# Kernel optimization log

Hardware: AMD Instinct MI355X
Metric: run time of the kernel (lower is better)

## Reference

```python
import jax, jax.numpy as jnp
import numpy as np

DIM = 256
GROUPS = 32
EPS = 1e-6


def setup_inputs() -> dict:
    key = jax.random.key(0)
    ks = jax.random.split(key, 7)
    B, C, H, W = 4, DIM, 64, 64
    s = 1.0 / np.sqrt(C)
    return {
        "x": jax.random.normal(ks[0], (B, C, H, W), dtype=jnp.float32),
        "gamma": jnp.ones((C,), dtype=jnp.float32),
        "beta": jnp.zeros((C,), dtype=jnp.float32),
        "w_qkv": jax.random.normal(ks[1], (3 * C, C), dtype=jnp.float32) * s,
        "b_qkv": jnp.zeros((3 * C,), dtype=jnp.float32),
        "w_proj": jax.random.normal(ks[2], (C, C), dtype=jnp.float32) * s,
        "b_proj": jnp.zeros((C,), dtype=jnp.float32),
    }


def reference(x, gamma, beta, w_qkv, b_qkv, w_proj, b_proj):
    B, C, H, W = x.shape
    N = H * W
    scale = jnp.asarray(C, x.dtype) ** 0.5

    # GroupNorm(32, C, eps=1e-6, affine)
    h = x.reshape(B, GROUPS, C // GROUPS, N)
    mu = h.mean(axis=(2, 3), keepdims=True)
    var = h.var(axis=(2, 3), keepdims=True)
    h = (h - mu) * jax.lax.rsqrt(var + EPS)
    h = h.reshape(B, C, N) * gamma[None, :, None] + beta[None, :, None]

    # 1x1 conv QKV == channel matmul
    qkv = jnp.einsum('oc,bcn->bon', w_qkv, h) + b_qkv[None, :, None]  # (B,3C,N)
    qkv = qkv.reshape(B, 3, C, N)
    q = qkv[:, 0].transpose(0, 2, 1)  # (B,N,C)
    k = qkv[:, 1].transpose(0, 2, 1)
    v = qkv[:, 2].transpose(0, 2, 1)

    attn = jnp.einsum('bqc,bkc->bqk', q, k) / scale  # (B,N,N)
    attn = jax.nn.softmax(attn, axis=-1)
    out = jnp.einsum('bqk,bkc->bqc', attn, v)  # (B,N,C)

    out = out.transpose(0, 2, 1)  # (B,C,N)
    out = jnp.einsum('oc,bcn->bon', w_proj, out) + b_proj[None, :, None]
    return x + out.reshape(B, C, H, W)
```

## Files before the change

kernel.cpp:

```cpp
#include <hip/hip_runtime.h>
#include <stdint.h>

#define DIM 256
#define NPOS 4096
#define NB 4
#define GROUPS 32

typedef __attribute__((ext_vector_type(8))) short short8;
typedef __attribute__((ext_vector_type(4))) short short4v;
typedef __attribute__((ext_vector_type(4))) float f32x4;
typedef __attribute__((ext_vector_type(2))) unsigned int u32x2;

__device__ __forceinline__ short f2b(float f) {
  unsigned u = __float_as_uint(f);
  unsigned r = (u + 0x7fffu + ((u >> 16) & 1u)) >> 16;
  return (short)r;
}

__global__ void k_convert_w(const float* __restrict__ wq, const float* __restrict__ wp,
                            short* __restrict__ wqb, short* __restrict__ wpb) {
  int i = blockIdx.x * 256 + threadIdx.x;
  if (i < 768 * 256) wqb[i] = f2b(wq[i]);
  if (i < 256 * 256) wpb[i] = f2b(wp[i]);
}

__global__ void k_gn_stats(const float* __restrict__ x, float* __restrict__ stats) {
  int bg = blockIdx.x;
  const float4* b4 = (const float4*)(x + (size_t)bg * 8 * NPOS);
  float s = 0.f, ss = 0.f;
  for (int i = threadIdx.x; i < 8192; i += 256) {
    float4 v = b4[i];
    s  += v.x + v.y + v.z + v.w;
    ss += v.x * v.x + v.y * v.y + v.z * v.z + v.w * v.w;
  }
  #pragma unroll
  for (int m = 1; m < 64; m <<= 1) { s += __shfl_xor(s, m, 64); ss += __shfl_xor(ss, m, 64); }
  __shared__ float red[8];
  int wid = threadIdx.x >> 6;
  if ((threadIdx.x & 63) == 0) { red[wid * 2] = s; red[wid * 2 + 1] = ss; }
  __syncthreads();
  if (threadIdx.x == 0) {
    float S = red[0] + red[2] + red[4] + red[6];
    float SS = red[1] + red[3] + red[5] + red[7];
    float mean = S / 32768.f;
    float var = SS / 32768.f - mean * mean;
    stats[bg * 2] = mean;
    stats[bg * 2 + 1] = rsqrtf(var + 1e-6f);
  }
}

__global__ void k_gn_apply(const float* __restrict__ x, const float* __restrict__ stats,
                           const float* __restrict__ gamma, const float* __restrict__ beta,
                           short* __restrict__ ht) {
  int ct = blockIdx.x, nt = blockIdx.y, b = blockIdx.z;
  int c0 = ct * 64, n0 = nt * 64;
  __shared__ short lt[64 * 72];
  int t = threadIdx.x;
  #pragma unroll
  for (int p = 0; p < 4; ++p) {
    int row = (t >> 4) + p * 16;
    int colb = (t & 15) * 4;
    int c = c0 + row;
    float mean = stats[(b * GROUPS + (c >> 3)) * 2];
    float rstd = stats[(b * GROUPS + (c >> 3)) * 2 + 1];
    float ga = gamma[c], be = beta[c];
    float4 v = *(const float4*)(x + ((size_t)(b * DIM + c)) * NPOS + n0 + colb);
    short4v o;
    o.x = f2b((v.x - mean) * rstd * ga + be);
    o.y = f2b((v.y - mean) * rstd * ga + be);
    o.z = f2b((v.z - mean) * rstd * ga + be);
    o.w = f2b((v.w - mean) * rstd * ga + be);
    *(short4v*)&lt[row * 72 + colb] = o;
  }
  __syncthreads();
  #pragma unroll
  for (int p = 0; p < 2; ++p) {
    int nr = (t >> 3) + p * 32;
    int ch = t & 7;
    short8 o;
    #pragma unroll
    for (int j = 0; j < 8; ++j) o[j] = lt[(ch * 8 + j) * 72 + nr];
    *(short8*)(ht + ((size_t)(b * NPOS + n0 + nr)) * DIM + c0 + ch * 8) = o;
  }
}

template <int MODE>
__launch_bounds__(256, 2)
__global__ void k_gemm(const short* __restrict__ A, const short* __restrict__ Bm,
                       const float* __restrict__ bias,
                       short* __restrict__ qb, short* __restrict__ kb, short* __restrict__ vtb,
                       const float* __restrict__ resid, float* __restrict__ outf) {
  const int K = 256;
  int b = blockIdx.z;
  int m0 = blockIdx.x * 128, n0 = blockIdx.y * 128;
  const short* Ap = (MODE == 0) ? A + (size_t)b * NPOS * K : A;
  const short* Bp = (MODE == 0) ? Bm : Bm + (size_t)b * NPOS * K;

  __shared__ short As[128 * 64], Bs[128 * 64];
  int t = threadIdx.x;
  int lane = t & 63, wid = t >> 6;
  int wm = wid >> 1, wn = wid & 1;
  f32x4 acc[4][4] = {};

  for (int kt = 0; kt < 4; ++kt) {
    int k0 = kt * 64;
    short8 av[4], bv[4];
    #pragma unroll
    for (int p = 0; p < 4; ++p) {
      int ci = t + p * 256;
      int row = ci >> 3, ch = ci & 7;
      av[p] = *(const short8*)(Ap + (size_t)(m0 + row) * K + k0 + ch * 8);
      bv[p] = *(const short8*)(Bp + (size_t)(n0 + row) * K + k0 + ch * 8);
    }
    __syncthreads();
    #pragma unroll
    for (int p = 0; p < 4; ++p) {
      int ci = t + p * 256;
      int row = ci >> 3, ch = ci & 7;
      int off = (row * 128 + ch * 16) ^ ((row & 7) << 4);
      *(short8*)((char*)As + off) = av[p];
      *(short8*)((char*)Bs + off) = bv[p];
    }
    __syncthreads();
    #pragma unroll
    for (int ks = 0; ks < 2; ++ks) {
      short8 af[4], bf[4];
      int inner = ks * 64 + (lane >> 4) * 16;
      #pragma unroll
      for (int mi = 0; mi < 4; ++mi) {
        int row = wm * 64 + mi * 16 + (lane & 15);
        af[mi] = *(short8*)((char*)As + ((row * 128 + inner) ^ ((row & 7) << 4)));
      }
      #pragma unroll
      for (int ni = 0; ni < 4; ++ni) {
        int row = wn * 64 + ni * 16 + (lane & 15);
        bf[ni] = *(short8*)((char*)Bs + ((row * 128 + inner) ^ ((row & 7) << 4)));
      }
      #pragma unroll
      for (int mi = 0; mi < 4; ++mi)
        #pragma unroll
        for (int ni = 0; ni < 4; ++ni)
          acc[mi][ni] = __builtin_amdgcn_mfma_f32_16x16x32_bf16(af[mi], bf[ni], acc[mi][ni], 0, 0, 0);
    }
  }

  #pragma unroll
  for (int mi = 0; mi < 4; ++mi)
    #pragma unroll
    for (int ni = 0; ni < 4; ++ni) {
      int gcol = n0 + wn * 64 + ni * 16 + (lane & 15);
      #pragma unroll
      for (int r = 0; r < 4; ++r) {
        int grow = m0 + wm * 64 + mi * 16 + (lane >> 4) * 4 + r;
        if (MODE == 0) {
          float v = acc[mi][ni][r] + bias[gcol];
          short h = f2b(v);
          if (gcol < 256)       qb[((size_t)b * NPOS + grow) * DIM + gcol] = h;
          else if (gcol < 512)  kb[((size_t)b * NPOS + grow) * DIM + gcol - 256] = h;
          else                  vtb[((size_t)b * DIM + gcol - 512) * NPOS + grow] = h;
        } else {
          float v = acc[mi][ni][r] + bias[grow];
          size_t idx = ((size_t)b * DIM + grow) * NPOS + gcol;
          outf[idx] = v + resid[idx];
        }
      }
    }
}

__launch_bounds__(256, 2)
__global__ void k_flash(const short* __restrict__ qb, const short* __restrict__ kb,
                        const short* __restrict__ vtb, short* __restrict__ ob) {
  __shared__ __align__(16) char smem[79360];

  int i = blockIdx.x;
  int xcd = i & 7, slot = i >> 3;
  int b = xcd >> 1;
  int bx = slot * 2 + (xcd & 1);
  int q0 = bx * 32;

  int t = threadIdx.x, lane = t & 63, g = lane >> 4, wid = t >> 6;
  int qs = wid & 1, h = wid >> 1;

  const short* kbB = kb + (size_t)b * NPOS * DIM;
  const short* vbB = vtb + (size_t)b * DIM * NPOS;

  short8 qf[8];
  {
    int qrow = q0 + qs * 16 + (lane & 15);
    const short* qp = qb + ((size_t)b * NPOS + qrow) * DIM + g * 8;
    #pragma unroll
    for (int s = 0; s < 8; ++s) {
      short8 v = *(const short8*)(qp + s * 32);
      #pragma unroll
      for (int j = 0; j < 8; ++j) {
        float f = __uint_as_float(((unsigned)(unsigned short)v[j]) << 16) * 0.0625f;
        v[j] = f2b(f);
      }
      qf[s] = v;
    }
  }

  const short* A0 = kbB + (t >> 5) * 256 + (t & 31) * 8;
  const short* B0 = vbB + (t >> 2) * 4096 + (t & 3) * 8;

  int krd = h * 16896 + (lane & 15) * 528 + g * 16;
  int vrd = 33792 + h * 20480 + (lane & 15) * 80 + g * 16;
  char* prow = smem + 74752 + wid * 1024 + (lane & 15) * 64;
  float* lm = (float*)(smem + 78848);
  float* scratch = (float*)smem;

  int kwr = (t >> 5) * 528 + (t & 31) * 16;
  int vwr = 33792 + (t >> 2) * 80 + (t & 3) * 16;

  f32x4 oacc[16] = {};
  float m = -1e30f, l = 0.f;

  short8 st[16];
  #pragma unroll
  for (int p = 0; p < 16; ++p) {
    int seg = p >> 2, pp = p & 3;
    if (seg < 2) st[p] = *(const short8*)(A0 + seg * 524288 + pp * 2048);
    else         st[p] = *(const short8*)(B0 + pp * 262144 + (seg - 2) * 2048);
  }

  const int NIT = 64;
  for (int it = 0; it < NIT; ++it) {
    __syncthreads();
    #pragma unroll
    for (int p = 0; p < 16; ++p) {
      int seg = p >> 2, pp = p & 3;
      if (seg < 2) *(short8*)(smem + seg * 16896 + pp * 4224 + kwr) = st[p];
      else         *(short8*)(smem + (seg - 2) * 20480 + pp * 5120 + vwr) = st[p];
    }
    __syncthreads();
    if (it + 1 < NIT) {
      #pragma unroll
      for (int p = 0; p < 16; ++p) {
        int seg = p >> 2, pp = p & 3;
        if (seg < 2) st[p] = *(const short8*)(A0 + seg * 524288 + pp * 2048 + (it + 1) * 8192);
        else         st[p] = *(const short8*)(B0 + pp * 262144 + (seg - 2) * 2048 + (it + 1) * 32);
      }
    }

    f32x4 sacc[2] = {};
    #pragma unroll
    for (int s = 0; s < 8; ++s) {
      #pragma unroll
      for (int t2 = 0; t2 < 2; ++t2) {
        short8 kf = *(short8*)(smem + krd + t2 * 8448 + s * 64);
        sacc[t2] = __builtin_amdgcn_mfma_f32_16x16x32_bf16(kf, qf[s], sacc[t2], 0, 0, 0);
      }
    }

    float mx = fmaxf(fmaxf(fmaxf(sacc[0][0], sacc[0][1]), fmaxf(sacc[0][2], sacc[0][3])),
                     fmaxf(fmaxf(sacc[1][0], sacc[1][1]), fmaxf(sacc[1][2], sacc[1][3])));
    mx = fmaxf(mx, __shfl_xor(mx, 16, 64));
    mx = fmaxf(mx, __shfl_xor(mx, 32, 64));
    if (!__all(mx <= m + 8.f)) {
      float mn = fmaxf(m, mx);
      float al = __expf(m - mn);
      m = mn; l *= al;
      #pragma unroll
      for (int r = 0; r < 4; ++r) {
        float ar = __shfl(al, (lane & 48) + ((lane & 48) >> 2) + r, 64);
        #pragma unroll
        for (int nt = 0; nt < 16; ++nt) oacc[nt][r] *= ar;
      }
    }
    float p0 = __expf(sacc[0][0] - m), p1 = __expf(sacc[0][1] - m);
    float p2 = __expf(sacc[0][2] - m), p3 = __expf(sacc[0][3] - m);
    float p4 = __expf(sacc[1][0] - m), p5 = __expf(sacc[1][1] - m);
    float p6 = __expf(sacc[1][2] - m), p7 = __expf(sacc[1][3] - m);
    float ts = ((p0 + p1) + (p2 + p3)) + ((p4 + p5) + (p6 + p7));
    ts += __shfl_xor(ts, 16, 64);
    ts += __shfl_xor(ts, 32, 64);
    l += ts;

    unsigned w0, w1, w2, w3;
    asm("v_cvt_pk_bf16_f32 %0, %1, %2" : "=v"(w0) : "v"(p0), "v"(p1));
    asm("v_cvt_pk_bf16_f32 %0, %1, %2" : "=v"(w1) : "v"(p2), "v"(p3));
    asm("v_cvt_pk_bf16_f32 %0, %1, %2" : "=v"(w2) : "v"(p4), "v"(p5));
    asm("v_cvt_pk_bf16_f32 %0, %1, %2" : "=v"(w3) : "v"(p6), "v"(p7));
    *(short4v*)(prow + g * 8)      = __builtin_bit_cast(short4v, (u32x2){w0, w1});
    *(short4v*)(prow + 32 + g * 8) = __builtin_bit_cast(short4v, (u32x2){w2, w3});
    asm volatile("" ::: "memory");

    short8 pa = *(short8*)(prow + g * 16);
    #pragma unroll
    for (int nt = 0; nt < 16; ++nt) {
      short8 vf = *(short8*)(smem + vrd + nt * 1280);
      oacc[nt] = __builtin_amdgcn_mfma_f32_16x16x32_bf16(pa, vf, oacc[nt], 0, 0, 0);
    }
  }

  __syncthreads();
  if (lane < 16) { lm[wid * 32 + lane * 2] = m; lm[wid * 32 + lane * 2 + 1] = l; }
  __syncthreads();
  int pw = wid ^ 2;
  float mo = lm[pw * 32 + (lane & 15) * 2];
  float lo = lm[pw * 32 + (lane & 15) * 2 + 1];
  float M = fmaxf(m, mo);
  float al = __expf(m - M);
  float Lf = l * al + lo * __expf(mo - M);
  float alr[4], iLr[4];
  #pragma unroll
  for (int r = 0; r < 4; ++r) {
    int src = (lane & 48) + ((lane & 48) >> 2) + r;
    alr[r] = __shfl(al, src, 64);
    iLr[r] = 1.f / __shfl(Lf, src, 64);
  }
  __syncthreads();
  if (h == 0) {
    float* sc = scratch + qs * 4096;
    #pragma unroll
    for (int nt = 0; nt < 16; ++nt)
      #pragma unroll
      for (int r = 0; r < 4; ++r) {
        int q = 4 * g + r;
        int col = nt * 16 + (lane & 15);
        sc[(q * 256 + col) ^ ((g & 1) << 4)] = oacc[nt][r] * alr[r];
      }
  }
  __syncthreads();
  if (h == 1) {
    float* sc = scratch + qs * 4096;
    #pragma unroll
    for (int nt = 0; nt < 16; ++nt)
      #pragma unroll
      for (int r = 0; r < 4; ++r) {
        int q = 4 * g + r;
        int col = nt * 16 + (lane & 15);
        float v = (sc[(q * 256 + col) ^ ((g & 1) << 4)] + oacc[nt][r] * alr[r]) * iLr[r];
        ob[((size_t)b * NPOS + q0 + qs * 16 + q) * DIM + col] = f2b(v);
      }
  }
}

extern "C" void kernel_launch(void* const* d_in, const int* in_sizes, int n_in,
                              void* d_out, int out_size, void* d_ws, size_t ws_size,
                              hipStream_t stream) {
  const float* x     = (const float*)d_in[0];
  const float* gamma = (const float*)d_in[1];
  const float* beta  = (const float*)d_in[2];
  const float* wqkv  = (const float*)d_in[3];
  const float* bqkv  = (const float*)d_in[4];
  const float* wproj = (const float*)d_in[5];
  const float* bproj = (const float*)d_in[6];
  float* out = (float*)d_out;

  char* ws = (char*)d_ws;
  float* stats = (float*)ws;
  short* wqb = (short*)(ws + 1024);
  short* wpb = (short*)(ws + 1024 + 393216);
  size_t off = 1024 + 393216 + 131072;
  const size_t SZ = (size_t)NB * NPOS * DIM * sizeof(short);
  short* ht   = (short*)(ws + off); off += SZ;
  short* qbuf = (short*)(ws + off); off += SZ;
  short* kbuf = (short*)(ws + off); off += SZ;
  short* vtb  = (short*)(ws + off); off += SZ;
  short* obuf = ht;

  k_convert_w<<<768, 256, 0, stream>>>(wqkv, wproj, wqb, wpb);
  k_gn_stats<<<128, 256, 0, stream>>>(x, stats);
  k_gn_apply<<<dim3(4, 64, NB), 256, 0, stream>>>(x, stats, gamma, beta, ht);
  k_gemm<0><<<dim3(32, 6, NB), 256, 0, stream>>>(ht, wqb, bqkv, qbuf, kbuf, vtb, nullptr, nullptr);
  k_flash<<<dim3(512), 256, 0, stream>>>(qbuf, kbuf, vtb, obuf);
  k_gemm<1><<<dim3(2, 32, NB), 256, 0, stream>>>(wpb, obuf, bproj, nullptr, nullptr, nullptr, x, out);
}
```

Baseline: 217.6 us.

## Load K/V fragments directly from global memory instead of staging through LDS

Drops the shared-memory staging of K and V tiles, along with the register prefetch and the two barriers per iteration. Each wave now reads its MFMA operand fragments for K and transposed V straight from global memory. This shrinks LDS use and removes barrier stalls, but loses the cross-wave reuse and the software prefetch. The loads become strided (16-byte pieces per row), and latency is hidden only by occupancy and the compiler's scheduling.

```diff
diff --git a/kernel.cpp b/kernel.cpp
--- a/kernel.cpp
+++ b/kernel.cpp
@@ -170,7 +170,9 @@
 __launch_bounds__(256, 2)
 __global__ void k_flash(const short* __restrict__ qb, const short* __restrict__ kb,
                         const short* __restrict__ vtb, short* __restrict__ ob) {
-  __shared__ __align__(16) char smem[79360];
+  __shared__ __align__(16) char smem[37376];
+  float* lm = (float*)(smem + 4096);
+  float* scratch = (float*)(smem + 4608);
 
   int i = blockIdx.x;
   int xcd = i & 7, slot = i >> 3;
@@ -200,56 +202,35 @@
     }
   }
 
-  const short* A0 = kbB + (t >> 5) * 256 + (t & 31) * 8;
-  const short* B0 = vbB + (t >> 2) * 4096 + (t & 3) * 8;
-
-  int krd = h * 16896 + (lane & 15) * 528 + g * 16;
-  int vrd = 33792 + h * 20480 + (lane & 15) * 80 + g * 16;
-  char* prow = smem + 74752 + wid * 1024 + (lane & 15) * 64;
-  float* lm = (float*)(smem + 78848);
-  float* scratch = (float*)smem;
-
-  int kwr = (t >> 5) * 528 + (t & 31) * 16;
-  int vwr = 33792 + (t >> 2) * 80 + (t & 3) * 16;
+  const short* kL = kbB + ((size_t)(h * 2048 + (lane & 15))) * DIM + g * 8;
+  const short* vL = vbB + ((size_t)(lane & 15)) * NPOS + h * 2048 + g * 8;
+  char* prow = smem + wid * 1024 + (lane & 15) * 64;
 
   f32x4 oacc[16] = {};
   float m = -1e30f, l = 0.f;
 
-  short8 st[16];
-  #pragma unroll
-  for (int p = 0; p < 16; ++p) {
-    int seg = p >> 2, pp = p & 3;
-    if (seg < 2) st[p] = *(const short8*)(A0 + seg * 524288 + pp * 2048);
-    else         st[p] = *(const short8*)(B0 + pp * 262144 + (seg - 2) * 2048);
-  }
-
   const int NIT = 64;
   for (int it = 0; it < NIT; ++it) {
-    __syncthreads();
-    #pragma unroll
-    for (int p = 0; p < 16; ++p) {
-      int seg = p >> 2, pp = p & 3;
-      if (seg < 2) *(short8*)(smem + seg * 16896 + pp * 4224 + kwr) = st[p];
-      else         *(short8*)(smem + (seg - 2) * 20480 + pp * 5120 + vwr) = st[p];
-    }
-    __syncthreads();
-    if (it + 1 < NIT) {
-      #pragma unroll
-      for (int p = 0; p < 16; ++p) {
-        int seg = p >> 2, pp = p & 3;
-        if (seg < 2) st[p] = *(const short8*)(A0 + seg * 524288 + pp * 2048 + (it + 1) * 8192);
-        else         st[p] = *(const short8*)(B0 + pp * 262144 + (seg - 2) * 2048 + (it + 1) * 32);
-      }
-    }
+    int kv0 = it * 32;
+
+    short8 kf[2][8];
+    #pragma unroll
+    for (int t2 = 0; t2 < 2; ++t2)
+      #pragma unroll
+      for (int s = 0; s < 8; ++s)
+        kf[t2][s] = *(const short8*)(kL + (size_t)(kv0 + t2 * 16) * DIM + s * 32);
+
+    short8 vf[16];
+    #pragma unroll
+    for (int nt = 0; nt < 16; ++nt)
+      vf[nt] = *(const short8*)(vL + (size_t)(nt * 16) * NPOS + kv0);
 
     f32x4 sacc[2] = {};
     #pragma unroll
     for (int s = 0; s < 8; ++s) {
       #pragma unroll
-      for (int t2 = 0; t2 < 2; ++t2) {
-        short8 kf = *(short8*)(smem + krd + t2 * 8448 + s * 64);
-        sacc[t2] = __builtin_amdgcn_mfma_f32_16x16x32_bf16(kf, qf[s], sacc[t2], 0, 0, 0);
-      }
+      for (int t2 = 0; t2 < 2; ++t2)
+        sacc[t2] = __builtin_amdgcn_mfma_f32_16x16x32_bf16(kf[t2][s], qf[s], sacc[t2], 0, 0, 0);
     }
 
     float mx = fmaxf(fmaxf(fmaxf(sacc[0][0], sacc[0][1]), fmaxf(sacc[0][2], sacc[0][3])),
@@ -287,10 +268,8 @@
 
     short8 pa = *(short8*)(prow + g * 16);
     #pragma unroll
-    for (int nt = 0; nt < 16; ++nt) {
-      short8 vf = *(short8*)(smem + vrd + nt * 1280);
-      oacc[nt] = __builtin_amdgcn_mfma_f32_16x16x32_bf16(pa, vf, oacc[nt], 0, 0, 0);
-    }
+    for (int nt = 0; nt < 16; ++nt)
+      oacc[nt] = __builtin_amdgcn_mfma_f32_16x16x32_bf16(pa, vf[nt], oacc[nt], 0, 0, 0);
   }
 
   __syncthreads();
@@ -309,7 +288,6 @@
     alr[r] = __shfl(al, src, 64);
     iLr[r] = 1.f / __shfl(Lf, src, 64);
   }
-  __syncthreads();
   if (h == 0) {
     float* sc = scratch + qs * 4096;
     #pragma unroll
```

Result: slower. 505.3 us (+132.2%).

## Double-buffer K/V via direct global-to-LDS loads and double query rows per block

Applied to the files above, without the earlier changes.

The flash kernel now moves K and V tiles straight into LDS with global_load_lds, double-buffered, with an XOR swizzle on the K layout. This replaces the register-staged copy and drops one barrier per iteration. Each wave now handles two 16-row query tiles, so every K/V fragment read from LDS feeds two MFMAs, and the grid is halved to 256 blocks. In exchange each block uses much more LDS and registers, occupancy falls to one block per CU, and fewer blocks are available for parallelism.

```diff
diff --git a/kernel.cpp b/kernel.cpp
--- a/kernel.cpp
+++ b/kernel.cpp
@@ -15,6 +15,11 @@
   unsigned u = __float_as_uint(f);
   unsigned r = (u + 0x7fffu + ((u >> 16) & 1u)) >> 16;
   return (short)r;
+}
+
+__device__ __forceinline__ void gl16(const short* g, char* lds) {
+  __builtin_amdgcn_global_load_lds((const __attribute__((address_space(1))) void*)g,
+                                   (__attribute__((address_space(3))) void*)lds, 16, 0, 0);
 }
 
 __global__ void k_convert_w(const float* __restrict__ wq, const float* __restrict__ wp,
@@ -167,26 +172,29 @@
     }
 }
 
-__launch_bounds__(256, 2)
+__launch_bounds__(256, 1)
 __global__ void k_flash(const short* __restrict__ qb, const short* __restrict__ kb,
                         const short* __restrict__ vtb, short* __restrict__ ob) {
-  __shared__ __align__(16) char smem[79360];
+  __shared__ __align__(16) char smem[140288];
+  float* lm = (float*)(smem + 139264);
+  float* scratch = (float*)smem;
 
   int i = blockIdx.x;
   int xcd = i & 7, slot = i >> 3;
   int b = xcd >> 1;
   int bx = slot * 2 + (xcd & 1);
-  int q0 = bx * 32;
-
-  int t = threadIdx.x, lane = t & 63, g = lane >> 4, wid = t >> 6;
+  int q0 = bx * 64;
+
+  int t = threadIdx.x, lane = t & 63, g = lane >> 4, q = lane & 15, wid = t >> 6;
   int qs = wid & 1, h = wid >> 1;
 
   const short* kbB = kb + (size_t)b * NPOS * DIM;
   const short* vbB = vtb + (size_t)b * DIM * NPOS;
 
-  short8 qf[8];
-  {
-    int qrow = q0 + qs * 16 + (lane & 15);
+  short8 qf[2][8];
+  #pragma unroll
+  for (int u = 0; u < 2; ++u) {
+    int qrow = q0 + qs * 32 + u * 16 + q;
     const short* qp = qb + ((size_t)b * NPOS + qrow) * DIM + g * 8;
     #pragma unroll
     for (int s = 0; s < 8; ++s) {
@@ -196,143 +204,167 @@
         float f = __uint_as_float(((unsigned)(unsigned short)v[j]) << 16) * 0.0625f;
         v[j] = f2b(f);
       }
-      qf[s] = v;
-    }
-  }
-
-  const short* A0 = kbB + (t >> 5) * 256 + (t & 31) * 8;
-  const short* B0 = vbB + (t >> 2) * 4096 + (t & 3) * 8;
-
-  int krd = h * 16896 + (lane & 15) * 528 + g * 16;
-  int vrd = 33792 + h * 20480 + (lane & 15) * 80 + g * 16;
-  char* prow = smem + 74752 + wid * 1024 + (lane & 15) * 64;
-  float* lm = (float*)(smem + 78848);
-  float* scratch = (float*)smem;
-
-  int kwr = (t >> 5) * 528 + (t & 31) * 16;
-  int vwr = 33792 + (t >> 2) * 80 + (t & 3) * 16;
-
-  f32x4 oacc[16] = {};
-  float m = -1e30f, l = 0.f;
-
-  short8 st[16];
-  #pragma unroll
-  for (int p = 0; p < 16; ++p) {
-    int seg = p >> 2, pp = p & 3;
-    if (seg < 2) st[p] = *(const short8*)(A0 + seg * 524288 + pp * 2048);
-    else         st[p] = *(const short8*)(B0 + pp * 262144 + (seg - 2) * 2048);
-  }
+      qf[u][s] = v;
+    }
+  }
+
+  unsigned su = h * 16384u + qs * 8192u;
+  const short* srcK[8];
+  const short* srcV[8];
+  {
+    int l5 = lane >> 5, l31 = lane & 31;
+    #pragma unroll
+    for (int j = 0; j < 8; ++j) {
+      int r = qs * 16 + j * 2 + l5;
+      int colb = (l31 * 16) ^ (((j * 2 + l5) & 7) << 4);
+      srcK[j] = kbB + (size_t)(h * 2048 + r) * DIM + (colb >> 1);
+      srcV[j] = vbB + (size_t)(qs * 128 + j * 16 + (lane >> 2)) * NPOS + h * 2048 + (lane & 3) * 8;
+    }
+  }
+
+  char* Pb = smem + 131072 + wid * 2048;
+  char* prow0 = Pb + q * 64;
+
+  f32x4 oacc[2][16] = {};
+  float mS[2] = {-1e30f, -1e30f}, lS[2] = {0.f, 0.f};
 
   const int NIT = 64;
+  int buf = 0;
+  #pragma unroll
+  for (int j = 0; j < 8; ++j) {
+    gl16(srcK[j], smem + su + j * 1024u);
+    gl16(srcV[j], smem + 65536u + su + j * 1024u);
+  }
+  __syncthreads();
+
   for (int it = 0; it < NIT; ++it) {
+    if (it + 1 < NIT) {
+      size_t ko = (size_t)(it + 1) * 32 * DIM;
+      int vo = (it + 1) * 32;
+      unsigned nb = (unsigned)(buf ^ 1) * 32768u + su;
+      #pragma unroll
+      for (int j = 0; j < 8; ++j) {
+        gl16(srcK[j] + ko, smem + nb + j * 1024u);
+        gl16(srcV[j] + vo, smem + 65536u + nb + j * 1024u);
+      }
+    }
+
+    const char* kl = smem + (unsigned)buf * 32768u + h * 16384u;
+    int xr = (q & 7) << 4;
+    f32x4 sacc[2][2] = {};
+    #pragma unroll
+    for (int s = 0; s < 8; ++s) {
+      #pragma unroll
+      for (int t2 = 0; t2 < 2; ++t2) {
+        short8 kf = *(const short8*)(kl + (t2 * 16 + q) * 512 + ((s * 64 + g * 16) ^ xr));
+        sacc[t2][0] = __builtin_amdgcn_mfma_f32_16x16x32_bf16(kf, qf[0][s], sacc[t2][0], 0, 0, 0);
+        sacc[t2][1] = __builtin_amdgcn_mfma_f32_16x16x32_bf16(kf, qf[1][s], sacc[t2][1], 0, 0, 0);
+      }
+    }
+
+    #pragma unroll
+    for (int u = 0; u < 2; ++u) {
+      float s0 = sacc[0][u][0], s1 = sacc[0][u][1], s2 = sacc[0][u][2], s3 = sacc[0][u][3];
+      float s4 = sacc[1][u][0], s5 = sacc[1][u][1], s6 = sacc[1][u][2], s7 = sacc[1][u][3];
+      float mx = fmaxf(fmaxf(fmaxf(s0, s1), fmaxf(s2, s3)), fmaxf(fmaxf(s4, s5), fmaxf(s6, s7)));
+      mx = fmaxf(mx, __shfl_xor(mx, 16, 64));
+      mx = fmaxf(mx, __shfl_xor(mx, 32, 64));
+      if (!__all(mx <= mS[u] + 8.f)) {
+        float mn = fmaxf(mS[u], mx);
+        float al = __expf(mS[u] - mn);
+        mS[u] = mn; lS[u] *= al;
+        #pragma unroll
+        for (int r = 0; r < 4; ++r) {
+          float ar = __shfl(al, (lane & 48) + ((lane & 48) >> 2) + r, 64);
+          #pragma unroll
+          for (int nt = 0; nt < 16; ++nt) oacc[u][nt][r] *= ar;
+        }
+      }
+      float p0 = __expf(s0 - mS[u]), p1 = __expf(s1 - mS[u]);
+      float p2 = __expf(s2 - mS[u]), p3 = __expf(s3 - mS[u]);
+      float p4 = __expf(s4 - mS[u]), p5 = __expf(s5 - mS[u]);
+      float p6 = __expf(s6 - mS[u]), p7 = __expf(s7 - mS[u]);
+      float ts = ((p0 + p1) + (p2 + p3)) + ((p4 + p5) + (p6 + p7));
+      ts += __shfl_xor(ts, 16, 64);
+      ts += __shfl_xor(ts, 32, 64);
+      lS[u] += ts;
+      unsigned w0, w1, w2, w3;
+      asm("v_cvt_pk_bf16_f32 %0, %1, %2" : "=v"(w0) : "v"(p0), "v"(p1));
+      asm("v_cvt_pk_bf16_f32 %0, %1, %2" : "=v"(w1) : "v"(p2), "v"(p3));
+      asm("v_cvt_pk_bf16_f32 %0, %1, %2" : "=v"(w2) : "v"(p4), "v"(p5));
+      asm("v_cvt_pk_bf16_f32 %0, %1, %2" : "=v"(w3) : "v"(p6), "v"(p7));
+      *(short4v*)(prow0 + u * 1024 + g * 8)      = __builtin_bit_cast(short4v, (u32x2){w0, w1});
+      *(short4v*)(prow0 + u * 1024 + 32 + g * 8) = __builtin_bit_cast(short4v, (u32x2){w2, w3});
+    }
+    asm volatile("" ::: "memory");
+
+    short8 pa0 = *(short8*)(prow0 + q * 0 + g * 16);
+    short8 pa1 = *(short8*)(prow0 + 1024 + g * 16);
+    const char* vl = smem + 65536u + (unsigned)buf * 32768u + h * 16384u;
+    #pragma unroll
+    for (int nt = 0; nt < 16; ++nt) {
+      short8 vf = *(const short8*)(vl + (nt * 16 + q) * 64 + g * 16);
+      oacc[0][nt] = __builtin_amdgcn_mfma_f32_16x16x32_bf16(pa0, vf, oacc[0][nt], 0, 0, 0);
+      oacc[1][nt] = __builtin_amdgcn_mfma_f32_16x16x32_bf16(pa1, vf, oacc[1][nt], 0, 0, 0);
+    }
     __syncthreads();
-    #pragma unroll
-    for (int p = 0; p < 16; ++p) {
-      int seg = p >> 2, pp = p & 3;
-      if (seg < 2) *(short8*)(smem + seg * 16896 + pp * 4224 + kwr) = st[p];
-      else         *(short8*)(smem + (seg - 2) * 20480 + pp * 5120 + vwr) = st[p];
-    }
-    __syncthreads();
-    if (it + 1 < NIT) {
-      #pragma unroll
-      for (int p = 0; p < 16; ++p) {
-        int seg = p >> 2, pp = p & 3;
-        if (seg < 2) st[p] = *(const short8*)(A0 + seg * 524288 + pp * 2048 + (it + 1) * 8192);
-        else         st[p] = *(const short8*)(B0 + pp * 262144 + (seg - 2) * 2048 + (it + 1) * 32);
-      }
-    }
-
-    f32x4 sacc[2] = {};
-    #pragma unroll
-    for (int s = 0; s < 8; ++s) {
-      #pragma unroll
-      for (int t2 = 0; t2 < 2; ++t2) {
-        short8 kf = *(short8*)(smem + krd + t2 * 8448 + s * 64);
-        sacc[t2] = __builtin_amdgcn_mfma_f32_16x16x32_bf16(kf, qf[s], sacc[t2], 0, 0, 0);
-      }
-    }
-
-    float mx = fmaxf(fmaxf(fmaxf(sacc[0][0], sacc[0][1]), fmaxf(sacc[0][2], sacc[0][3])),
-                     fmaxf(fmaxf(sacc[1][0], sacc[1][1]), fmaxf(sacc[1][2], sacc[1][3])));
-    mx = fmaxf(mx, __shfl_xor(mx, 16, 64));
-    mx = fmaxf(mx, __shfl_xor(mx, 32, 64));
-    if (!__all(mx <= m + 8.f)) {
-      float mn = fmaxf(m, mx);
-      float al = __expf(m - mn);
-      m = mn; l *= al;
-      #pragma unroll
-      for (int r = 0; r < 4; ++r) {
-        float ar = __shfl(al, (lane & 48) + ((lane & 48) >> 2) + r, 64);
+    buf ^= 1;
+  }
+
+  if (lane < 16) {
+    #pragma unroll
+    for (int u = 0; u < 2; ++u) {
+      lm[(wid * 32 + u * 16 + lane) * 2]     = mS[u];
+      lm[(wid * 32 + u * 16 + lane) * 2 + 1] = lS[u];
+    }
+  }
+  __syncthreads();
+  int pw = wid ^ 2;
+  float alr[2][4], iLr[2][4];
+  #pragma unroll
+  for (int u = 0; u < 2; ++u) {
+    float mo = lm[(pw * 32 + u * 16 + q) * 2];
+    float lo = lm[(pw * 32 + u * 16 + q) * 2 + 1];
+    float M = fmaxf(mS[u], mo);
+    float al = __expf(mS[u] - M);
+    float Lf = lS[u] * al + lo * __expf(mo - M);
+    #pragma unroll
+    for (int r = 0; r < 4; ++r) {
+      int src = (lane & 48) + ((lane & 48) >> 2) + r;
+      alr[u][r] = __shfl(al, src, 64);
+      iLr[u][r] = 1.f / __shfl(Lf, src, 64);
+    }
+  }
+  __syncthreads();
+  if (h == 0) {
+    #pragma unroll
+    for (int u = 0; u < 2; ++u) {
+      float* sc = scratch + (qs * 2 + u) * 4096;
+      #pragma unroll
+      for (int nt = 0; nt < 16; ++nt)
         #pragma unroll
-        for (int nt = 0; nt < 16; ++nt) oacc[nt][r] *= ar;
-      }
-    }
-    float p0 = __expf(sacc[0][0] - m), p1 = __expf(sacc[0][1] - m);
-    float p2 = __expf(sacc[0][2] - m), p3 = __expf(sacc[0][3] - m);
-    float p4 = __expf(sacc[1][0] - m), p5 = __expf(sacc[1][1] - m);
-    float p6 = __expf(sacc[1][2] - m), p7 = __expf(sacc[1][3] - m);
-    float ts = ((p0 + p1) + (p2 + p3)) + ((p4 + p5) + (p6 + p7));
-    ts += __shfl_xor(ts, 16, 64);
-    ts += __shfl_xor(ts, 32, 64);
-    l += ts;
-
-    unsigned w0, w1, w2, w3;
-    asm("v_cvt_pk_bf16_f32 %0, %1, %2" : "=v"(w0) : "v"(p0), "v"(p1));
-    asm("v_cvt_pk_bf16_f32 %0, %1, %2" : "=v"(w1) : "v"(p2), "v"(p3));
-    asm("v_cvt_pk_bf16_f32 %0, %1, %2" : "=v"(w2) : "v"(p4), "v"(p5));
-    asm("v_cvt_pk_bf16_f32 %0, %1, %2" : "=v"(w3) : "v"(p6), "v"(p7));
-    *(short4v*)(prow + g * 8)      = __builtin_bit_cast(short4v, (u32x2){w0, w1});
-    *(short4v*)(prow + 32 + g * 8) = __builtin_bit_cast(short4v, (u32x2){w2, w3});
-    asm volatile("" ::: "memory");
-
-    short8 pa = *(short8*)(prow + g * 16);
-    #pragma unroll
-    for (int nt = 0; nt < 16; ++nt) {
-      short8 vf = *(short8*)(smem + vrd + nt * 1280);
-      oacc[nt] = __builtin_amdgcn_mfma_f32_16x16x32_bf16(pa, vf, oacc[nt], 0, 0, 0);
-    }
-  }
-
-  __syncthreads();
-  if (lane < 16) { lm[wid * 32 + lane * 2] = m; lm[wid * 32 + lane * 2 + 1] = l; }
-  __syncthreads();
-  int pw = wid ^ 2;
-  float mo = lm[pw * 32 + (lane & 15) * 2];
-  float lo = lm[pw * 32 + (lane & 15) * 2 + 1];
-  float M = fmaxf(m, mo);
-  float al = __expf(m - M);
-  float Lf = l * al + lo * __expf(mo - M);
-  float alr[4], iLr[4];
-  #pragma unroll
-  for (int r = 0; r < 4; ++r) {
-    int src = (lane & 48) + ((lane & 48) >> 2) + r;
-    alr[r] = __shfl(al, src, 64);
-    iLr[r] = 1.f / __shfl(Lf, src, 64);
-  }
-  __syncthreads();
-  if (h == 0) {
-    float* sc = scratch + qs * 4096;
-    #pragma unroll
-    for (int nt = 0; nt < 16; ++nt)
-      #pragma unroll
-      for (int r = 0; r < 4; ++r) {
-        int q = 4 * g + r;
-        int col = nt * 16 + (lane & 15);
-        sc[(q * 256 + col) ^ ((g & 1) << 4)] = oacc[nt][r] * alr[r];
-      }
+        for (int r = 0; r < 4; ++r) {
+          int ql = 4 * g + r;
+          int col = nt * 16 + q;
+          sc[(ql * 256 + col) ^ ((g & 1) << 4)] = oacc[u][nt][r] * alr[u][r];
+        }
+    }
   }
   __syncthreads();
   if (h == 1) {
-    float* sc = scratch + qs * 4096;
-    #pragma unroll
-    for (int nt = 0; nt < 16; ++nt)
-      #pragma unroll
-      for (int r = 0; r < 4; ++r) {
-        int q = 4 * g + r;
-        int col = nt * 16 + (lane & 15);
-        float v = (sc[(q * 256 + col) ^ ((g & 1) << 4)] + oacc[nt][r] * alr[r]) * iLr[r];
-        ob[((size_t)b * NPOS + q0 + qs * 16 + q) * DIM + col] = f2b(v);
-      }
+    #pragma unroll
+    for (int u = 0; u < 2; ++u) {
+      float* sc = scratch + (qs * 2 + u) * 4096;
+      #pragma unroll
+      for (int nt = 0; nt < 16; ++nt)
+        #pragma unroll
+        for (int r = 0; r < 4; ++r) {
+          int ql = 4 * g + r;
+          int col = nt * 16 + q;
+          float v = (sc[(ql * 256 + col) ^ ((g & 1) << 4)] + oacc[u][nt][r] * alr[u][r]) * iLr[u][r];
+          ob[((size_t)b * NPOS + q0 + qs * 32 + u * 16 + ql) * DIM + col] = f2b(v);
+        }
+    }
   }
 }
 
@@ -364,6 +396,6 @@
   k_gn_stats<<<128, 256, 0, stream>>>(x, stats);
   k_gn_apply<<<dim3(4, 64, NB), 256, 0, stream>>>(x, stats, gamma, beta, ht);
   k_gemm<0><<<dim3(32, 6, NB), 256, 0, stream>>>(ht, wqb, bqkv, qbuf, kbuf, vtb, nullptr, nullptr);
-  k_flash<<<dim3(512), 256, 0, stream>>>(qbuf, kbuf, vtb, obuf);
+  k_flash<<<dim3(256), 256, 0, stream>>>(qbuf, kbuf, vtb, obuf);
   k_gemm<1><<<dim3(2, 32, NB), 256, 0, stream>>>(wpb, obuf, bproj, nullptr, nullptr, nullptr, x, out);
 }
```

Result: faster. 200.5 us (-7.8%).
